# Kernel tuning notes

Measured on AMD Instinct MI355X. Metric: run time of the kernel, lower is better.

Reference implementation:

```python
import jax, jax.numpy as jnp
import numpy as np

VOCAB = 50000
DIM = 768


def setup_inputs() -> dict:
    key = jax.random.key(0)
    k1, k2, k3, k4 = jax.random.split(key, 4)
    token = jax.random.randint(k1, (32, 512), 0, VOCAB, dtype=jnp.int64)
    need_mapper = jax.random.randint(k2, (VOCAB,), 0, 2, dtype=jnp.int32)
    bert_embedding = jax.random.normal(k3, (VOCAB, DIM), dtype=jnp.float32)
    mapper_w = jax.random.normal(k4, (DIM, DIM), dtype=jnp.float32) * (1.0 / np.sqrt(DIM))
    mapper_b = jnp.zeros((DIM,), dtype=jnp.float32)
    return {
        "token": token,
        "need_mapper": need_mapper,
        "bert_embedding": bert_embedding,
        "mapper_w": mapper_w,
        "mapper_b": mapper_b,
    }


def reference(token, need_mapper, bert_embedding, mapper_w, mapper_b):
    # Gather: [B, S, D] -- irregular access into the embedding table.
    vecs = bert_embedding[token]
    # Conditional mapper (vectorized over all tokens; selected by per-id mask).
    mapped = jnp.einsum("bsd,de->bse", vecs, mapper_w) + mapper_b
    need = need_mapper[token].astype(bool)  # [B, S]
    return jnp.where(need[..., None], mapped, vecs)
```

## Files before the change

### kernel.cpp

```cpp
#include <hip/hip_runtime.h>
#include <hip/hip_bf16.h>
#include <stdint.h>
#include <stddef.h>

#define DIM 768

typedef short short8 __attribute__((ext_vector_type(8)));
typedef float f32x4 __attribute__((ext_vector_type(4)));

__device__ inline unsigned short f2bf_rne(float f) {
    union { float f; unsigned u; } x; x.f = f;
    unsigned r = x.u + 0x7fffu + ((x.u >> 16) & 1u);
    return (unsigned short)(r >> 16);
}

__device__ inline void gload_lds16(const void* g, void* l) {
    __builtin_amdgcn_global_load_lds((const __attribute__((address_space(1))) void*)g,
                                     (__attribute__((address_space(3))) void*)l, 16, 0, 0);
}

__global__ __launch_bounds__(256) void convw_kernel(
    const float* __restrict__ w, unsigned short* __restrict__ Bt)
{
    __shared__ unsigned short t[64][65];
    const int k0 = blockIdx.x * 64, n0 = blockIdx.y * 64;
    const int tid = threadIdx.x;
#pragma unroll
    for (int p = 0; p < 16; ++p) {
        int e = p * 256 + tid;
        int r = e >> 6, c = e & 63;
        t[c][r] = f2bf_rne(w[(size_t)(k0 + r) * DIM + n0 + c]);
    }
    __syncthreads();
#pragma unroll
    for (int p = 0; p < 16; ++p) {
        int e = p * 256 + tid;
        int r = e >> 6, c = e & 63;
        Bt[(size_t)(n0 + r) * DIM + k0 + c] = t[r][c];
    }
}

__global__ __launch_bounds__(256) void fused_gemm_kernel(
    const int* __restrict__ token,
    const int* __restrict__ need_mapper,
    const float* __restrict__ emb,
    const unsigned short* __restrict__ Bt,
    const float* __restrict__ bias,
    float* __restrict__ out)
{
    __shared__ float As[128 * 32];
    __shared__ unsigned short Bs[128 * 32];
    __shared__ int tok_s[128];
    __shared__ int flag_s[128];

    const int tid  = threadIdx.x;
    const int wave = tid >> 6;
    const int lane = tid & 63;
    const int quad = lane >> 4;
    const int l15  = lane & 15;
    const int wm   = wave >> 1;
    const int wn   = wave & 1;
    const int tile_m = blockIdx.x;
    const int tile_n = blockIdx.y;

    if (tid < 128) {
        int t = token[tile_m * 128 + tid];
        tok_s[tid]  = t;
        flag_s[tid] = need_mapper[t];
    }
    __syncthreads();

    const int r8 = tid >> 3;
    const int c8 = tid & 7;
    const float* pA[4];
#pragma unroll
    for (int j = 0; j < 4; ++j) {
        int r = j * 32 + r8;
        pA[j] = emb + (size_t)tok_s[r] * DIM + ((c8 ^ (r & 7)) << 2);
    }
    float* lA0 = As + (wave * 8) * 32;
    const unsigned short* pB = Bt + (size_t)(tile_n * 128 + (tid >> 2)) * DIM + (tid & 3) * 8;
    unsigned short* lB = Bs + wave * 512;

    f32x4 acc[4][4] = {};

    for (int kk = 0; kk < DIM; kk += 32) {
        __syncthreads();
#pragma unroll
        for (int j = 0; j < 4; ++j)
            gload_lds16(pA[j] + kk, lA0 + j * 32 * 32);
        gload_lds16(pB + kk,                   lB);
        gload_lds16(pB + kk + (size_t)64 * DIM, lB + 2048);
        __syncthreads();

        short8 af[4], bf[4];
#pragma unroll
        for (int i = 0; i < 4; ++i) {
            const int m = wm * 64 + i * 16 + l15;
            const float* row = As + (m << 5);
            f32x4 a0 = *(const f32x4*)(row + ((((quad << 1)    ) ^ (m & 7)) << 2));
            f32x4 a1 = *(const f32x4*)(row + ((((quad << 1) + 1) ^ (m & 7)) << 2));
            unsigned u0 = __float_as_uint(a0[0]) + 0x8000u;
            unsigned u1 = __float_as_uint(a0[1]) + 0x8000u;
            unsigned u2 = __float_as_uint(a0[2]) + 0x8000u;
            unsigned u3 = __float_as_uint(a0[3]) + 0x8000u;
            unsigned u4 = __float_as_uint(a1[0]) + 0x8000u;
            unsigned u5 = __float_as_uint(a1[1]) + 0x8000u;
            unsigned u6 = __float_as_uint(a1[2]) + 0x8000u;
            unsigned u7 = __float_as_uint(a1[3]) + 0x8000u;
            union { int i4[4]; short8 s; } pk;
            pk.i4[0] = __builtin_amdgcn_perm(u1, u0, 0x07060302);
            pk.i4[1] = __builtin_amdgcn_perm(u3, u2, 0x07060302);
            pk.i4[2] = __builtin_amdgcn_perm(u5, u4, 0x07060302);
            pk.i4[3] = __builtin_amdgcn_perm(u7, u6, 0x07060302);
            af[i] = pk.s;
        }
#pragma unroll
        for (int j = 0; j < 4; ++j)
            bf[j] = *(const short8*)(Bs + (wn * 64 + j * 16 + l15) * 32 + quad * 8);
#pragma unroll
        for (int i = 0; i < 4; ++i)
#pragma unroll
            for (int j = 0; j < 4; ++j)
                acc[i][j] = __builtin_amdgcn_mfma_f32_16x16x32_bf16(af[i], bf[j], acc[i][j], 0, 0, 0);
    }

    const int colg = tile_n * 128 + wn * 64 + l15;
    float bv[4];
#pragma unroll
    for (int j = 0; j < 4; ++j) bv[j] = bias[colg + j * 16];

#pragma unroll
    for (int i = 0; i < 4; ++i) {
#pragma unroll
        for (int r = 0; r < 4; ++r) {
            const int lrow = wm * 64 + i * 16 + quad * 4 + r;
            const int gm   = tile_m * 128 + lrow;
            float* orow = out + (size_t)gm * DIM + colg;
            if (flag_s[lrow]) {
#pragma unroll
                for (int j = 0; j < 4; ++j)
                    orow[j * 16] = acc[i][j][r] + bv[j];
            } else {
                const float* erow = emb + (size_t)tok_s[lrow] * DIM + colg;
#pragma unroll
                for (int j = 0; j < 4; ++j)
                    orow[j * 16] = erow[j * 16];
            }
        }
    }
}

extern "C" void kernel_launch(void* const* d_in, const int* in_sizes, int n_in,
                              void* d_out, int out_size, void* d_ws, size_t ws_size,
                              hipStream_t stream)
{
    const int*   token       = (const int*)d_in[0];
    const int*   need_mapper = (const int*)d_in[1];
    const float* emb         = (const float*)d_in[2];
    const float* w           = (const float*)d_in[3];
    const float* bias        = (const float*)d_in[4];
    float* out = (float*)d_out;

    const int ntok = in_sizes[0];

    unsigned short* Bt = (unsigned short*)d_ws;

    convw_kernel<<<dim3(DIM / 64, DIM / 64), dim3(256), 0, stream>>>(w, Bt);
    fused_gemm_kernel<<<dim3(ntok / 128, DIM / 128), dim3(256), 0, stream>>>(
        token, need_mapper, emb, Bt, bias, out);
}
```

Measured before the change: 242.8 us.

## Stage full bf16 gathered rows in LDS once and loop over all N tiles

Each block now owns 32 tokens, gathers their full 768-wide embedding rows once, converts them to bf16 and keeps them resident in LDS (48KB). It then iterates over three 256-column N tiles, streaming only the weight tile per K step. Before, the 128x128 tiling re-read the fp32 gathered rows for each of 6 N tiles. The aim is to cut the redundant random gathers and fp32 LDS traffic. In exchange the grid grows to 512 blocks with fewer MFMAs per B load, and the large LDS footprint limits occupancy.

```diff
diff --git a/kernel.cpp b/kernel.cpp
--- a/kernel.cpp
+++ b/kernel.cpp
@@ -40,7 +40,7 @@
     }
 }
 
-__global__ __launch_bounds__(256) void fused_gemm_kernel(
+__global__ __launch_bounds__(256, 2) void fused_gemm_kernel(
     const int* __restrict__ token,
     const int* __restrict__ need_mapper,
     const float* __restrict__ emb,
@@ -48,104 +48,109 @@
     const float* __restrict__ bias,
     float* __restrict__ out)
 {
-    __shared__ float As[128 * 32];
-    __shared__ unsigned short Bs[128 * 32];
-    __shared__ int tok_s[128];
-    __shared__ int flag_s[128];
+    __shared__ unsigned short As[32 * DIM];
+    __shared__ unsigned short Bs[256 * 32];
 
     const int tid  = threadIdx.x;
     const int wave = tid >> 6;
     const int lane = tid & 63;
     const int quad = lane >> 4;
     const int l15  = lane & 15;
-    const int wm   = wave >> 1;
-    const int wn   = wave & 1;
-    const int tile_m = blockIdx.x;
-    const int tile_n = blockIdx.y;
+    const int m0   = blockIdx.x * 32;
 
-    if (tid < 128) {
-        int t = token[tile_m * 128 + tid];
-        tok_s[tid]  = t;
-        flag_s[tid] = need_mapper[t];
-    }
-    __syncthreads();
-
-    const int r8 = tid >> 3;
-    const int c8 = tid & 7;
-    const float* pA[4];
 #pragma unroll
-    for (int j = 0; j < 4; ++j) {
-        int r = j * 32 + r8;
-        pA[j] = emb + (size_t)tok_s[r] * DIM + ((c8 ^ (r & 7)) << 2);
-    }
-    float* lA0 = As + (wave * 8) * 32;
-    const unsigned short* pB = Bt + (size_t)(tile_n * 128 + (tid >> 2)) * DIM + (tid & 3) * 8;
-    unsigned short* lB = Bs + wave * 512;
-
-    f32x4 acc[4][4] = {};
-
-    for (int kk = 0; kk < DIM; kk += 32) {
-        __syncthreads();
-#pragma unroll
-        for (int j = 0; j < 4; ++j)
-            gload_lds16(pA[j] + kk, lA0 + j * 32 * 32);
-        gload_lds16(pB + kk,                   lB);
-        gload_lds16(pB + kk + (size_t)64 * DIM, lB + 2048);
-        __syncthreads();
-
-        short8 af[4], bf[4];
-#pragma unroll
-        for (int i = 0; i < 4; ++i) {
-            const int m = wm * 64 + i * 16 + l15;
-            const float* row = As + (m << 5);
-            f32x4 a0 = *(const f32x4*)(row + ((((quad << 1)    ) ^ (m & 7)) << 2));
-            f32x4 a1 = *(const f32x4*)(row + ((((quad << 1) + 1) ^ (m & 7)) << 2));
-            unsigned u0 = __float_as_uint(a0[0]) + 0x8000u;
-            unsigned u1 = __float_as_uint(a0[1]) + 0x8000u;
-            unsigned u2 = __float_as_uint(a0[2]) + 0x8000u;
-            unsigned u3 = __float_as_uint(a0[3]) + 0x8000u;
-            unsigned u4 = __float_as_uint(a1[0]) + 0x8000u;
-            unsigned u5 = __float_as_uint(a1[1]) + 0x8000u;
-            unsigned u6 = __float_as_uint(a1[2]) + 0x8000u;
-            unsigned u7 = __float_as_uint(a1[3]) + 0x8000u;
-            union { int i4[4]; short8 s; } pk;
-            pk.i4[0] = __builtin_amdgcn_perm(u1, u0, 0x07060302);
-            pk.i4[1] = __builtin_amdgcn_perm(u3, u2, 0x07060302);
-            pk.i4[2] = __builtin_amdgcn_perm(u5, u4, 0x07060302);
-            pk.i4[3] = __builtin_amdgcn_perm(u7, u6, 0x07060302);
-            af[i] = pk.s;
-        }
-#pragma unroll
-        for (int j = 0; j < 4; ++j)
-            bf[j] = *(const short8*)(Bs + (wn * 64 + j * 16 + l15) * 32 + quad * 8);
-#pragma unroll
-        for (int i = 0; i < 4; ++i)
-#pragma unroll
-            for (int j = 0; j < 4; ++j)
-                acc[i][j] = __builtin_amdgcn_mfma_f32_16x16x32_bf16(af[i], bf[j], acc[i][j], 0, 0, 0);
+    for (int it = 0; it < 12; ++it) {
+        int e = it * 256 + tid;
+        int r = e / 96;
+        int q = e - r * 96;
+        int p = (q & ~7) | ((q & 7) ^ (r & 7));
+        int tok = token[m0 + r];
+        const float* src = emb + (size_t)tok * DIM + q * 8;
+        float4 v0 = *(const float4*)src;
+        float4 v1 = *(const float4*)(src + 4);
+        unsigned u0 = __float_as_uint(v0.x) + 0x8000u;
+        unsigned u1 = __float_as_uint(v0.y) + 0x8000u;
+        unsigned u2 = __float_as_uint(v0.z) + 0x8000u;
+        unsigned u3 = __float_as_uint(v0.w) + 0x8000u;
+        unsigned u4 = __float_as_uint(v1.x) + 0x8000u;
+        unsigned u5 = __float_as_uint(v1.y) + 0x8000u;
+        unsigned u6 = __float_as_uint(v1.z) + 0x8000u;
+        unsigned u7 = __float_as_uint(v1.w) + 0x8000u;
+        union { int i4[4]; short8 s; } pk;
+        pk.i4[0] = __builtin_amdgcn_perm(u1, u0, 0x07060302);
+        pk.i4[1] = __builtin_amdgcn_perm(u3, u2, 0x07060302);
+        pk.i4[2] = __builtin_amdgcn_perm(u5, u4, 0x07060302);
+        pk.i4[3] = __builtin_amdgcn_perm(u7, u6, 0x07060302);
+        *(short8*)(As + r * DIM + p * 8) = pk.s;
     }
 
-    const int colg = tile_n * 128 + wn * 64 + l15;
-    float bv[4];
+    int tokr[2][4], flg[2][4];
 #pragma unroll
-    for (int j = 0; j < 4; ++j) bv[j] = bias[colg + j * 16];
+    for (int i = 0; i < 2; ++i)
+#pragma unroll
+        for (int r2 = 0; r2 < 4; ++r2) {
+            int row = i * 16 + quad * 4 + r2;
+            int t = token[m0 + row];
+            tokr[i][r2] = t;
+            flg[i][r2]  = need_mapper[t];
+        }
+
+    for (int n0 = 0; n0 < DIM; n0 += 256) {
+        f32x4 acc[2][4] = {};
+
+        for (int kk = 0; kk < DIM; kk += 32) {
+            __syncthreads();
+#pragma unroll
+            for (int j = 0; j < 4; ++j) {
+                int nloc = (tid >> 2) + 64 * j;
+                int q = (tid & 3) ^ ((nloc >> 1) & 3);
+                gload_lds16(Bt + (size_t)(n0 + nloc) * DIM + kk + q * 8,
+                            (char*)Bs + wave * 1024 + j * 4096);
+            }
+            __syncthreads();
+
+            short8 af[2], bf[4];
+#pragma unroll
+            for (int i = 0; i < 2; ++i) {
+                int r = i * 16 + l15;
+                int q = (kk >> 3) + quad;
+                int p = q ^ (r & 7);
+                af[i] = *(const short8*)(As + r * DIM + p * 8);
+            }
+#pragma unroll
+            for (int j = 0; j < 4; ++j) {
+                int nl = wave * 64 + j * 16 + l15;
+                int p = quad ^ ((nl >> 1) & 3);
+                bf[j] = *(const short8*)(Bs + nl * 32 + p * 8);
+            }
+#pragma unroll
+            for (int i = 0; i < 2; ++i)
+#pragma unroll
+                for (int j = 0; j < 4; ++j)
+                    acc[i][j] = __builtin_amdgcn_mfma_f32_16x16x32_bf16(af[i], bf[j], acc[i][j], 0, 0, 0);
+        }
+
+        const int colg = n0 + wave * 64 + l15;
+        float bv[4];
+#pragma unroll
+        for (int j = 0; j < 4; ++j) bv[j] = bias[colg + j * 16];
 
 #pragma unroll
-    for (int i = 0; i < 4; ++i) {
+        for (int i = 0; i < 2; ++i) {
 #pragma unroll
-        for (int r = 0; r < 4; ++r) {
-            const int lrow = wm * 64 + i * 16 + quad * 4 + r;
-            const int gm   = tile_m * 128 + lrow;
-            float* orow = out + (size_t)gm * DIM + colg;
-            if (flag_s[lrow]) {
+            for (int r2 = 0; r2 < 4; ++r2) {
+                int gm = m0 + i * 16 + quad * 4 + r2;
+                float* orow = out + (size_t)gm * DIM + colg;
+                if (flg[i][r2]) {
 #pragma unroll
-                for (int j = 0; j < 4; ++j)
-                    orow[j * 16] = acc[i][j][r] + bv[j];
-            } else {
-                const float* erow = emb + (size_t)tok_s[lrow] * DIM + colg;
+                    for (int j = 0; j < 4; ++j)
+                        orow[j * 16] = acc[i][j][r2] + bv[j];
+                } else {
+                    const float* erow = emb + (size_t)tokr[i][r2] * DIM + colg;
 #pragma unroll
-                for (int j = 0; j < 4; ++j)
-                    orow[j * 16] = erow[j * 16];
+                    for (int j = 0; j < 4; ++j)
+                        orow[j * 16] = erow[j * 16];
+                }
             }
         }
     }
@@ -167,6 +172,6 @@
     unsigned short* Bt = (unsigned short*)d_ws;
 
     convw_kernel<<<dim3(DIM / 64, DIM / 64), dim3(256), 0, stream>>>(w, Bt);
-    fused_gemm_kernel<<<dim3(ntok / 128, DIM / 128), dim3(256), 0, stream>>>(
+    fused_gemm_kernel<<<dim3(ntok / 32), dim3(256), 0, stream>>>(
         token, need_mapper, emb, Bt, bias, out);
 }
```

Result: slower. 270.5 us (+11.4%).
